# Kernel optimization log

Measured on AMD Instinct MI355X. Metric: run time of the kernel, lower is better.

Reference implementation:

```python
import jax, jax.numpy as jnp
import numpy as np

GRID_N = 256          # hardcoded 256x256 grid in the module
D = 64                # conv channel width
NL = 18               # module applications used (9 conv + 9 PReLU, interleaved)
LABEL_NC = 19
STYLE_DIM = 512


def setup_inputs() -> dict:
    key = jax.random.key(0)
    ks = jax.random.split(key, 7)
    B, C = 2, LABEL_NC
    x = jax.random.randint(ks[0], (B, C, GRID_N, GRID_N), 0, 2).astype(jnp.int32)
    conv_w0 = jax.random.normal(ks[1], (D, 2), dtype=jnp.float32) * 0.1
    conv_w = jax.random.normal(ks[2], (8, D, D), dtype=jnp.float32) * 0.05
    conv_b = jax.random.normal(ks[3], (9, D), dtype=jnp.float32) * 0.01
    prelu_a = jnp.full((9, D), 0.25, dtype=jnp.float32)  # PReLU default init
    fc_w = jax.random.normal(ks[4], (NL, STYLE_DIM, D * C), dtype=jnp.float32)
    fc_b = jnp.zeros((NL, STYLE_DIM), dtype=jnp.float32)
    return dict(x=x, conv_w0=conv_w0, conv_w=conv_w, conv_b=conv_b,
                prelu_a=prelu_a, fc_w=fc_w, fc_b=fc_b)


def _point_features(pts, conv_w0, conv_w, conv_b, prelu_a):
    """pts: (P,2). Returns (NL, P, D): snapshot after each of the 18 modules
    (conv, prelu, conv, prelu, ...) -- exactly what the original max-pools."""
    snaps = []
    z = pts @ conv_w0.T + conv_b[0]            # Conv1d(2,64,1) == pointwise linear
    snaps.append(z)
    z = jnp.where(z > 0, z, prelu_a[0] * z)    # PReLU(64)
    snaps.append(z)
    for i in range(8):
        z = z @ conv_w[i].T + conv_b[i + 1]
        snaps.append(z)
        z = jnp.where(z > 0, z, prelu_a[i + 1] * z)
        snaps.append(z)
    return jnp.stack(snaps)                    # (18, P, D)


def reference(x, conv_w0, conv_w, conv_b, prelu_a, fc_w, fc_b):
    B, C = x.shape[0], x.shape[1]
    P = GRID_N * GRID_N
    lin = jnp.linspace(-1.0, 1.0, GRID_N, dtype=jnp.float32)
    gx, gy = jnp.meshgrid(lin, lin)            # numpy default 'xy' indexing
    pts = jnp.stack([gx.reshape(-1), gy.reshape(-1)], axis=-1)   # (P, 2)

    # Grid points are shared by every (b, c): compute features once.
    snaps = _point_features(pts, conv_w0, conv_w, conv_b, prelu_a)        # (18, P, D)
    zero_snaps = _point_features(jnp.zeros((1, 2), jnp.float32),
                                 conv_w0, conv_w, conv_b, prelu_a)[:, 0]  # (18, D)

    mask = (x.reshape(B, C, P) == 1)           # (B, C, P)
    empty = ~jnp.any(mask, axis=-1)            # (B, C): original falls back to a zero point

    neg = jnp.float32(-jnp.inf)
    pooled = []
    for l in range(NL):                        # fixed, small layer loop
        pl = jnp.max(jnp.where(mask[..., None], snaps[l][None, None], neg), axis=2)  # (B,C,D)
        pl = jnp.where(empty[..., None], zero_snaps[l][None, None], pl)
        pooled.append(pl)
    pooled = jnp.stack(pooled, axis=1)         # (B, 18, C, D)
    feat = pooled.reshape(B, NL, C * D)        # channel-major concat, matches torch.cat dim=2

    # EqualLinear: out = x @ (W * scale).T + bias, scale = 1/sqrt(in_dim), lr_mul=1
    scale = 1.0 / jnp.sqrt(jnp.float32(C * D))
    # fcs are applied in reversed layer order and concatenated in that order
    w_rev = fc_w[::-1] * scale                 # (18, 512, C*D)
    b_rev = fc_b[::-1]                         # (18, 512)
    out = jnp.einsum('bld,lsd->bls', feat[:, ::-1], w_rev) + b_rev[None]
    return out                                  # (B, 18, 512)
```

## Files before the change

### kernel.cpp

```cpp
#include <hip/hip_runtime.h>
#include <hip/hip_fp16.h>

#define NSET 38
#define NSNAP 9
#define PART (NSNAP*NSET*64)
#define PPB 64
#define HSTR 72
#define PSTR 72
#define WHALF (8*64*64)

typedef unsigned int uint;
typedef __fp16 h2 __attribute__((ext_vector_type(2)));
typedef __fp16 h4 __attribute__((ext_vector_type(4)));
typedef __fp16 h8 __attribute__((ext_vector_type(8)));
typedef float  f32x4 __attribute__((ext_vector_type(4)));

#define HNEGINF 0xFC00u

static __device__ __forceinline__ h2 h2max(h2 a, h2 b) {
  return __builtin_elementwise_max(a, b);
}
#define SPLIT8(v, v0, v1, v2, v3)                       \
  h2 v0 = __builtin_shufflevector(v, v, 0, 1);          \
  h2 v1 = __builtin_shufflevector(v, v, 2, 3);          \
  h2 v2 = __builtin_shufflevector(v, v, 4, 5);          \
  h2 v3 = __builtin_shufflevector(v, v, 6, 7);

template<int CHUNKS>
__global__ __launch_bounds__(256)
void kA(const int* __restrict__ x, const float* __restrict__ w0,
        const float* __restrict__ cw, const float* __restrict__ cb,
        const float* __restrict__ pa, const __fp16* __restrict__ wf,
        __fp16* __restrict__ partialh)
{
  __shared__ __align__(16) __fp16 zth[PPB * HSTR];
  __shared__ __align__(16) __fp16 ztpA[64 * PSTR];
  __shared__ __align__(16) __fp16 ztpB[64 * PSTR];
  __shared__ __align__(16) __fp16 addp[40 * 64];
  __shared__ uint memb2[PPB * 2];

  const int tid = threadIdx.x;
  const int q  = tid & 63;
  const int g  = __builtin_amdgcn_readfirstlane(tid >> 6);
  const int lr = tid & 15;
  const int lg = (tid & 63) >> 4;
  const int sbase = g * 10;
  const int nset = (g == 3) ? 8 : 10;
  const __fp16 HNI = __builtin_bit_cast(__fp16, (unsigned short)0xFC00);
  const h2 H2NI = {HNI, HNI};

  auto prelu_frag = [&](int sv, f32x4* C, __fp16* ztpX) {
    #pragma unroll
    for (int dt = 0; dt < 4; ++dt) {
      int dim = (dt << 4) + lr;
      float a = pa[(sv << 6) + dim];
      __fp16 zp[4];
      #pragma unroll
      for (int r = 0; r < 4; ++r) {
        float zv = C[dt][r];
        zp[r] = (__fp16)(zv > 0.f ? zv : a * zv);
        zth[((g << 4) + (lg << 2) + r) * HSTR + dim] = zp[r];
      }
      int pt0 = (g << 4) + (lg << 2);
      h4 w4 = {zp[0], zp[1], zp[2], zp[3]};
      *(h4*)&ztpX[dim * PSTR + pt0] = w4;
    }
  };
  auto mfma_layer = [&](int sv, f32x4* C) {
    h8 a0 = *(const h8*)&zth[((g << 4) + lr) * HSTR + (lg << 3)];
    h8 a1 = *(const h8*)&zth[((g << 4) + lr) * HSTR + 32 + (lg << 3)];
    const __fp16* wb = wf + ((size_t)sv << 12);
    #pragma unroll
    for (int dt = 0; dt < 4; ++dt) {
      float bias = cb[((sv + 1) << 6) + (dt << 4) + lr];
      f32x4 a4 = {bias, bias, bias, bias};
      h8 b0 = *(const h8*)&wb[(((dt << 4) + lr) << 6) + (lg << 3)];
      h8 b1 = *(const h8*)&wb[(((dt << 4) + lr) << 6) + 32 + (lg << 3)];
      a4 = __builtin_amdgcn_mfma_f32_16x16x32_f16(a0, b0, a4, 0, 0, 0);
      a4 = __builtin_amdgcn_mfma_f32_16x16x32_f16(a1, b1, a4, 0, 0, 0);
      C[dt] = a4;
    }
  };
  auto fold_store = [&](int sv, h2* runv, int c) {
    __fp16* pb = partialh + (size_t)blockIdx.x * PART + sv * (NSET * 64) + q;
    #pragma unroll
    for (int j = 0; j < 10; ++j) {
      if (j < nset) {
        h2 r = runv[j];
        __fp16 m = r.x > r.y ? r.x : r.y;
        int off = (sbase + j) * 64;
        if (CHUNKS == 1 || c == 0) pb[off] = m;
        else { __fp16 o = pb[off]; pb[off] = (m > o) ? m : o; }
      }
    }
  };

  #pragma unroll 1
  for (int c = 0; c < CHUNKS; ++c) {
    const int p = (blockIdx.x * CHUNKS + c) * PPB + q;

    if (c) __syncthreads();
    if (tid < 128) {
      const int half = tid >> 6;
      uint m = 0;
      #pragma unroll
      for (int j = 0; j < 19; ++j)
        m |= (uint)(x[(half * 19 + j) * 65536 + p] == 1) << j;
      memb2[q * 2 + half] = m;
    }
    __syncthreads();

    {
      uint* addp32 = (uint*)addp;
      #pragma unroll
      for (int i = tid; i < 1280; i += 256) {
        int j = i >> 5, pr = i & 31;
        uint lo0 = memb2[(2 * pr) * 2],     hi0 = memb2[(2 * pr) * 2 + 1];
        uint lo1 = memb2[(2 * pr + 1) * 2], hi1 = memb2[(2 * pr + 1) * 2 + 1];
        uint b0 = (j < 19) ? ((lo0 >> j) & 1u) : (j < 38) ? ((hi0 >> (j - 19)) & 1u) : 0u;
        uint b1 = (j < 19) ? ((lo1 >> j) & 1u) : (j < 38) ? ((hi1 >> (j - 19)) & 1u) : 0u;
        addp32[i] = (b0 ? 0u : HNEGINF) | ((b1 ? 0u : HNEGINF) << 16);
      }
    }

    float acc0[16];
    {
      float px = -1.f + (2.f / 255.f) * (float)(p & 255);
      float py = -1.f + (2.f / 255.f) * (float)(p >> 8);
      #pragma unroll
      for (int d = 0; d < 16; ++d) {
        int dd = (g << 4) + d;
        acc0[d] = fmaf(px, w0[2 * dd], fmaf(py, w0[2 * dd + 1], cb[dd]));
      }
    }
    __syncthreads();

    #pragma unroll
    for (int d = 0; d < 16; ++d) {
      int dd = (g << 4) + d;
      float zv = acc0[d];
      float a = pa[dd];
      __fp16 zp = (__fp16)(zv > 0.f ? zv : a * zv);
      zth[q * HSTR + dd] = zp;
      ztpA[dd * PSTR + q] = zp;
    }
    __syncthreads();

    f32x4 Cf[4], Cf2[4];
    mfma_layer(0, Cf);

    {
      h2 runA[10];
      #pragma unroll
      for (int j = 0; j < 10; ++j) runA[j] = H2NI;
      #pragma unroll 2
      for (int c4 = 0; c4 < 8; ++c4) {
        h8 va = *(const h8*)&ztpA[q * PSTR + (c4 << 3)];
        SPLIT8(va, va0, va1, va2, va3)
        #pragma unroll
        for (int j = 0; j < 10; ++j) {
          h8 a8 = *(const h8*)&addp[((sbase + j) << 6) + (c4 << 3)];
          SPLIT8(a8, a0, a1, a2, a3)
          runA[j] = h2max(runA[j],
                     h2max(h2max(va0 + a0, va1 + a1), h2max(va2 + a2, va3 + a3)));
        }
      }
      fold_store(0, runA, c);
    }

    #pragma unroll 1
    for (int sp = 0; sp < 4; ++sp) {
      const int s = 1 + 2 * sp;
      __syncthreads();
      prelu_frag(s, Cf, ztpA);
      mfma_layer(s, Cf2);
      prelu_frag(s + 1, Cf2, ztpB);
      if (sp < 3) mfma_layer(s + 1, Cf);
      __syncthreads();

      h2 runA[10], runB[10];
      #pragma unroll
      for (int j = 0; j < 10; ++j) { runA[j] = H2NI; runB[j] = H2NI; }
      #pragma unroll 2
      for (int c4 = 0; c4 < 8; ++c4) {
        h8 va = *(const h8*)&ztpA[q * PSTR + (c4 << 3)];
        h8 vb = *(const h8*)&ztpB[q * PSTR + (c4 << 3)];
        SPLIT8(va, va0, va1, va2, va3)
        SPLIT8(vb, vb0, vb1, vb2, vb3)
        #pragma unroll
        for (int j = 0; j < 10; ++j) {
          h8 a8 = *(const h8*)&addp[((sbase + j) << 6) + (c4 << 3)];
          SPLIT8(a8, a0, a1, a2, a3)
          runA[j] = h2max(runA[j],
                     h2max(h2max(va0 + a0, va1 + a1), h2max(va2 + a2, va3 + a3)));
          runB[j] = h2max(runB[j],
                     h2max(h2max(vb0 + a0, vb1 + a1), h2max(vb2 + a2, vb3 + a3)));
        }
      }
      fold_store(s, runA, c);
      fold_store(s + 1, runB, c);
    }
  }
}

__global__ __launch_bounds__(256) void kW(const float* __restrict__ cw,
                                          __fp16* __restrict__ wf)
{
  int i = blockIdx.x * 256 + threadIdx.x;
  if (i < WHALF) wf[i] = (__fp16)cw[i];
}

__global__ __launch_bounds__(256) void kB1(const __fp16* __restrict__ ph,
    float* __restrict__ buf32, int per)
{
  int idx = blockIdx.x * 256 + threadIdx.x;
  if (idx >= PART) return;
  const __fp16* p0 = ph + (size_t)blockIdx.y * per * PART + idx;
  float mx = -3e38f;
  #pragma unroll 8
  for (int b = 0; b < per; ++b)
    mx = fmaxf(mx, (float)p0[(size_t)b * PART]);
  buf32[(size_t)blockIdx.y * PART + idx] = mx;
}

__global__ __launch_bounds__(256) void kB2(const float* __restrict__ buf32,
    const float* __restrict__ cw, const float* __restrict__ cb,
    const float* __restrict__ pa, float* __restrict__ feat)
{
  __shared__ float zl[64];
  __shared__ float zc[NSNAP][64];
  __shared__ float zp[NSNAP][64];
  int tid = threadIdx.x;
  int d = tid & 63;
  float z = cb[d];
  #pragma unroll 1
  for (int s = 0; s < NSNAP; ++s) {
    if (tid < 64) {
      zc[s][d] = z;
      float a = pa[(s << 6) + d];
      float v = z > 0.f ? z : a * z;
      zp[s][d] = v;
      zl[d] = v;
    }
    __syncthreads();
    if (s < 8) {
      if (tid < 64) {
        float a2 = cb[((s + 1) << 6) + d];
        for (int k = 0; k < 64; ++k)
          a2 = fmaf(zl[k], cw[(s << 12) + (d << 6) + k], a2);
        z = a2;
      }
    }
    __syncthreads();
  }

  int idx = blockIdx.x * 256 + tid;
  if (idx >= PART) return;
  int s = idx / (NSET * 64);
  int r = idx - s * (NSET * 64);
  int set = r >> 6;
  int dd = r & 63;
  float mx = -3e38f;
  #pragma unroll
  for (int y = 0; y < 32; ++y)
    mx = fmaxf(mx, buf32[(size_t)y * PART + idx]);
  int b = set / 19, cc = set - b * 19;
  float even_v, odd_v;
  if (mx < -5e37f) {
    even_v = zc[s][dd];
    odd_v  = zp[s][dd];
  } else {
    odd_v = mx;
    float a = pa[(s << 6) + dd];
    even_v = mx > 0.f ? mx : mx / a;
  }
  size_t fb = ((size_t)b * 18 + 2 * s) * 1216 + cc * 64 + dd;
  feat[fb] = even_v;
  feat[fb + 1216] = odd_v;
}

__global__ __launch_bounds__(256) void kC(const float* __restrict__ feat,
    const float* __restrict__ fcw, const float* __restrict__ fcb,
    float* __restrict__ out)
{
  __shared__ float f0[1216], f1[1216];
  int lr = blockIdx.y;
  int chunk = blockIdx.x;
  int tid = threadIdx.x;
  for (int i = tid; i < 1216; i += 256) {
    f0[i] = feat[(size_t)(0 * 18 + lr) * 1216 + i];
    f1[i] = feat[(size_t)(1 * 18 + lr) * 1216 + i];
  }
  __syncthreads();
  int wv = tid >> 6, lane = tid & 63;
  float scale = 1.f / sqrtf(1216.f);
  int l = 17 - lr;
  #pragma unroll 1
  for (int rr = 0; rr < 4; ++rr) {
    int srow = (chunk << 4) + (wv << 2) + rr;
    const float* wrow = fcw + ((size_t)lr * 512 + srow) * 1216;
    float pp0 = 0.f, pp1 = 0.f;
    #pragma unroll
    for (int k = 0; k < 19; ++k) {
      float w = wrow[(k << 6) + lane];
      pp0 = fmaf(w, f0[(k << 6) + lane], pp0);
      pp1 = fmaf(w, f1[(k << 6) + lane], pp1);
    }
    #pragma unroll
    for (int off = 32; off; off >>= 1) {
      pp0 += __shfl_xor(pp0, off, 64);
      pp1 += __shfl_xor(pp1, off, 64);
    }
    if (lane == 0) {
      float b = fcb[lr * 512 + srow];
      out[((size_t)0 * 18 + l) * 512 + srow] = fmaf(scale, pp0, b);
      out[((size_t)1 * 18 + l) * 512 + srow] = fmaf(scale, pp1, b);
    }
  }
}

extern "C" void kernel_launch(void* const* d_in, const int* in_sizes, int n_in,
                              void* d_out, int out_size, void* d_ws, size_t ws_size,
                              hipStream_t stream) {
  const int*   x   = (const int*)d_in[0];
  const float* w0  = (const float*)d_in[1];
  const float* cw  = (const float*)d_in[2];
  const float* cb  = (const float*)d_in[3];
  const float* pa  = (const float*)d_in[4];
  const float* fcw = (const float*)d_in[5];
  const float* fcb = (const float*)d_in[6];
  float* out = (float*)d_out;
  char* base = (char*)d_ws;

  #define NEED(n) ((size_t)(n) * PART * 2 + (size_t)32 * PART * 4 \
                   + (size_t)2 * 18 * 1216 * 4 + (size_t)WHALF * 2)

  int nblk;
  if      (ws_size >= NEED(1024)) nblk = 1024;
  else if (ws_size >= NEED(512))  nblk = 512;
  else                            nblk = 256;

  __fp16* partialh = (__fp16*)base;
  float*  buf32 = (float*)(base + (size_t)nblk * PART * 2);
  float*  feat  = buf32 + (size_t)32 * PART;
  __fp16* wf    = (__fp16*)(feat + (size_t)2 * 18 * 1216);
  const int per = nblk >> 5;

  hipLaunchKernelGGL(kW, dim3(WHALF / 256), dim3(256), 0, stream, cw, wf);

  if (nblk == 1024) {
    hipLaunchKernelGGL(kA<1>, dim3(1024), dim3(256), 0, stream,
                       x, w0, cw, cb, pa, wf, partialh);
  } else if (nblk == 512) {
    hipLaunchKernelGGL(kA<2>, dim3(512), dim3(256), 0, stream,
                       x, w0, cw, cb, pa, wf, partialh);
  } else {
    hipLaunchKernelGGL(kA<4>, dim3(256), dim3(256), 0, stream,
                       x, w0, cw, cb, pa, wf, partialh);
  }

  hipLaunchKernelGGL(kB1, dim3(86, 32), dim3(256), 0, stream,
                     partialh, buf32, per);
  hipLaunchKernelGGL(kB2, dim3(86), dim3(256), 0, stream,
                     buf32, cw, cb, pa, feat);
  hipLaunchKernelGGL(kC, dim3(32, 18), dim3(256), 0, stream, feat, fcw, fcb, out);
}
```

Baseline: 133.3 us.

## Pool three snapshots per pass with packed-f16 asm and grid-stride chunks

```diff
diff --git a/kernel.cpp b/kernel.cpp
--- a/kernel.cpp
+++ b/kernel.cpp
@@ -5,28 +5,31 @@
 #define NSNAP 9
 #define PART (NSNAP*NSET*64)
 #define PPB 64
+#define NCHUNK 1024
 #define HSTR 72
 #define PSTR 72
 #define WHALF (8*64*64)
 
 typedef unsigned int uint;
-typedef __fp16 h2 __attribute__((ext_vector_type(2)));
-typedef __fp16 h4 __attribute__((ext_vector_type(4)));
 typedef __fp16 h8 __attribute__((ext_vector_type(8)));
 typedef float  f32x4 __attribute__((ext_vector_type(4)));
 
 #define HNEGINF 0xFC00u
-
-static __device__ __forceinline__ h2 h2max(h2 a, h2 b) {
-  return __builtin_elementwise_max(a, b);
-}
-#define SPLIT8(v, v0, v1, v2, v3)                       \
-  h2 v0 = __builtin_shufflevector(v, v, 0, 1);          \
-  h2 v1 = __builtin_shufflevector(v, v, 2, 3);          \
-  h2 v2 = __builtin_shufflevector(v, v, 4, 5);          \
-  h2 v3 = __builtin_shufflevector(v, v, 6, 7);
-
-template<int CHUNKS>
+#define NEGPACK (HNEGINF | (HNEGINF << 16))
+
+static __device__ __forceinline__ uint pk_add(uint a, uint b) {
+  uint r; asm("v_pk_add_f16 %0, %1, %2" : "=v"(r) : "v"(a), "v"(b)); return r;
+}
+static __device__ __forceinline__ void pk_max_acc(uint& acc, uint t) {
+  asm("v_pk_max_f16 %0, %1, %0" : "+v"(acc) : "v"(t));
+}
+static __device__ __forceinline__ float half_lo_f(uint u) {
+  return (float)__builtin_bit_cast(__fp16, (unsigned short)(u & 0xFFFFu));
+}
+static __device__ __forceinline__ float half_hi_f(uint u) {
+  return (float)__builtin_bit_cast(__fp16, (unsigned short)(u >> 16));
+}
+
 __global__ __launch_bounds__(256)
 void kA(const int* __restrict__ x, const float* __restrict__ w0,
         const float* __restrict__ cw, const float* __restrict__ cb,
@@ -36,6 +39,7 @@
   __shared__ __align__(16) __fp16 zth[PPB * HSTR];
   __shared__ __align__(16) __fp16 ztpA[64 * PSTR];
   __shared__ __align__(16) __fp16 ztpB[64 * PSTR];
+  __shared__ __align__(16) __fp16 ztpC[64 * PSTR];
   __shared__ __align__(16) __fp16 addp[40 * 64];
   __shared__ uint memb2[PPB * 2];
 
@@ -46,8 +50,6 @@
   const int lg = (tid & 63) >> 4;
   const int sbase = g * 10;
   const int nset = (g == 3) ? 8 : 10;
-  const __fp16 HNI = __builtin_bit_cast(__fp16, (unsigned short)0xFC00);
-  const h2 H2NI = {HNI, HNI};
 
   auto prelu_frag = [&](int sv, f32x4* C, __fp16* ztpX) {
     #pragma unroll
@@ -62,8 +64,12 @@
         zth[((g << 4) + (lg << 2) + r) * HSTR + dim] = zp[r];
       }
       int pt0 = (g << 4) + (lg << 2);
-      h4 w4 = {zp[0], zp[1], zp[2], zp[3]};
-      *(h4*)&ztpX[dim * PSTR + pt0] = w4;
+      uint2 w2;
+      w2.x = (uint)__builtin_bit_cast(unsigned short, zp[0]) |
+             ((uint)__builtin_bit_cast(unsigned short, zp[1]) << 16);
+      w2.y = (uint)__builtin_bit_cast(unsigned short, zp[2]) |
+             ((uint)__builtin_bit_cast(unsigned short, zp[3]) << 16);
+      *(uint2*)&ztpX[dim * PSTR + pt0] = w2;
     }
   };
   auto mfma_layer = [&](int sv, f32x4* C) {
@@ -81,25 +87,57 @@
       C[dt] = a4;
     }
   };
-  auto fold_store = [&](int sv, h2* runv, int c) {
+  auto fold_store = [&](int sv, uint* runv, bool first) {
     __fp16* pb = partialh + (size_t)blockIdx.x * PART + sv * (NSET * 64) + q;
     #pragma unroll
     for (int j = 0; j < 10; ++j) {
       if (j < nset) {
-        h2 r = runv[j];
-        __fp16 m = r.x > r.y ? r.x : r.y;
+        __fp16 lo = __builtin_bit_cast(__fp16, (unsigned short)(runv[j] & 0xFFFFu));
+        __fp16 hi = __builtin_bit_cast(__fp16, (unsigned short)(runv[j] >> 16));
+        __fp16 m = lo > hi ? lo : hi;
         int off = (sbase + j) * 64;
-        if (CHUNKS == 1 || c == 0) pb[off] = m;
+        if (first) pb[off] = m;
         else { __fp16 o = pb[off]; pb[off] = (m > o) ? m : o; }
       }
     }
   };
+  auto pool3 = [&](int sa, bool first) {
+    uint runA[10], runB[10], runC[10];
+    #pragma unroll
+    for (int j = 0; j < 10; ++j) { runA[j] = NEGPACK; runB[j] = NEGPACK; runC[j] = NEGPACK; }
+    #pragma unroll 2
+    for (int c4 = 0; c4 < 8; ++c4) {
+      uint4 va = *(const uint4*)&ztpA[q * PSTR + (c4 << 3)];
+      uint4 vb = *(const uint4*)&ztpB[q * PSTR + (c4 << 3)];
+      uint4 vc = *(const uint4*)&ztpC[q * PSTR + (c4 << 3)];
+      #pragma unroll
+      for (int j = 0; j < 10; ++j) {
+        uint4 aj = *(const uint4*)&addp[((sbase + j) << 6) + (c4 << 3)];
+        pk_max_acc(runA[j], pk_add(va.x, aj.x));
+        pk_max_acc(runA[j], pk_add(va.y, aj.y));
+        pk_max_acc(runA[j], pk_add(va.z, aj.z));
+        pk_max_acc(runA[j], pk_add(va.w, aj.w));
+        pk_max_acc(runB[j], pk_add(vb.x, aj.x));
+        pk_max_acc(runB[j], pk_add(vb.y, aj.y));
+        pk_max_acc(runB[j], pk_add(vb.z, aj.z));
+        pk_max_acc(runB[j], pk_add(vb.w, aj.w));
+        pk_max_acc(runC[j], pk_add(vc.x, aj.x));
+        pk_max_acc(runC[j], pk_add(vc.y, aj.y));
+        pk_max_acc(runC[j], pk_add(vc.z, aj.z));
+        pk_max_acc(runC[j], pk_add(vc.w, aj.w));
+      }
+    }
+    fold_store(sa, runA, first);
+    fold_store(sa + 1, runB, first);
+    fold_store(sa + 2, runC, first);
+  };
 
   #pragma unroll 1
-  for (int c = 0; c < CHUNKS; ++c) {
-    const int p = (blockIdx.x * CHUNKS + c) * PPB + q;
-
-    if (c) __syncthreads();
+  for (int cid = blockIdx.x; cid < NCHUNK; cid += gridDim.x) {
+    const bool first = (cid == (int)blockIdx.x);
+    const int p = cid * PPB + q;
+
+    if (!first) __syncthreads();
     if (tid < 128) {
       const int half = tid >> 6;
       uint m = 0;
@@ -146,60 +184,33 @@
     }
     __syncthreads();
 
-    f32x4 Cf[4], Cf2[4];
-    mfma_layer(0, Cf);
-
-    {
-      h2 runA[10];
-      #pragma unroll
-      for (int j = 0; j < 10; ++j) runA[j] = H2NI;
-      #pragma unroll 2
-      for (int c4 = 0; c4 < 8; ++c4) {
-        h8 va = *(const h8*)&ztpA[q * PSTR + (c4 << 3)];
-        SPLIT8(va, va0, va1, va2, va3)
-        #pragma unroll
-        for (int j = 0; j < 10; ++j) {
-          h8 a8 = *(const h8*)&addp[((sbase + j) << 6) + (c4 << 3)];
-          SPLIT8(a8, a0, a1, a2, a3)
-          runA[j] = h2max(runA[j],
-                     h2max(h2max(va0 + a0, va1 + a1), h2max(va2 + a2, va3 + a3)));
-        }
-      }
-      fold_store(0, runA, c);
-    }
-
-    #pragma unroll 1
-    for (int sp = 0; sp < 4; ++sp) {
-      const int s = 1 + 2 * sp;
-      __syncthreads();
-      prelu_frag(s, Cf, ztpA);
-      mfma_layer(s, Cf2);
-      prelu_frag(s + 1, Cf2, ztpB);
-      if (sp < 3) mfma_layer(s + 1, Cf);
-      __syncthreads();
-
-      h2 runA[10], runB[10];
-      #pragma unroll
-      for (int j = 0; j < 10; ++j) { runA[j] = H2NI; runB[j] = H2NI; }
-      #pragma unroll 2
-      for (int c4 = 0; c4 < 8; ++c4) {
-        h8 va = *(const h8*)&ztpA[q * PSTR + (c4 << 3)];
-        h8 vb = *(const h8*)&ztpB[q * PSTR + (c4 << 3)];
-        SPLIT8(va, va0, va1, va2, va3)
-        SPLIT8(vb, vb0, vb1, vb2, vb3)
-        #pragma unroll
-        for (int j = 0; j < 10; ++j) {
-          h8 a8 = *(const h8*)&addp[((sbase + j) << 6) + (c4 << 3)];
-          SPLIT8(a8, a0, a1, a2, a3)
-          runA[j] = h2max(runA[j],
-                     h2max(h2max(va0 + a0, va1 + a1), h2max(va2 + a2, va3 + a3)));
-          runB[j] = h2max(runB[j],
-                     h2max(h2max(vb0 + a0, vb1 + a1), h2max(vb2 + a2, vb3 + a3)));
-        }
-      }
-      fold_store(s, runA, c);
-      fold_store(s + 1, runB, c);
-    }
+    f32x4 CfA[4], CfB[4];
+    mfma_layer(0, CfA);
+    prelu_frag(1, CfA, ztpB);
+    mfma_layer(1, CfB);
+    prelu_frag(2, CfB, ztpC);
+    mfma_layer(2, CfA);
+    __syncthreads();
+    pool3(0, first);
+
+    __syncthreads();
+    prelu_frag(3, CfA, ztpA);
+    mfma_layer(3, CfB);
+    prelu_frag(4, CfB, ztpB);
+    mfma_layer(4, CfA);
+    prelu_frag(5, CfA, ztpC);
+    mfma_layer(5, CfB);
+    __syncthreads();
+    pool3(3, first);
+
+    __syncthreads();
+    prelu_frag(6, CfB, ztpA);
+    mfma_layer(6, CfA);
+    prelu_frag(7, CfA, ztpB);
+    mfma_layer(7, CfB);
+    prelu_frag(8, CfB, ztpC);
+    __syncthreads();
+    pool3(6, first);
   }
 }
 
@@ -336,9 +347,9 @@
                    + (size_t)2 * 18 * 1216 * 4 + (size_t)WHALF * 2)
 
   int nblk;
-  if      (ws_size >= NEED(1024)) nblk = 1024;
-  else if (ws_size >= NEED(512))  nblk = 512;
-  else                            nblk = 256;
+  if      (ws_size >= NEED(768)) nblk = 768;
+  else if (ws_size >= NEED(512)) nblk = 512;
+  else                           nblk = 256;
 
   __fp16* partialh = (__fp16*)base;
   float*  buf32 = (float*)(base + (size_t)nblk * PART * 2);
@@ -347,18 +358,8 @@
   const int per = nblk >> 5;
 
   hipLaunchKernelGGL(kW, dim3(WHALF / 256), dim3(256), 0, stream, cw, wf);
-
-  if (nblk == 1024) {
-    hipLaunchKernelGGL(kA<1>, dim3(1024), dim3(256), 0, stream,
-                       x, w0, cw, cb, pa, wf, partialh);
-  } else if (nblk == 512) {
-    hipLaunchKernelGGL(kA<2>, dim3(512), dim3(256), 0, stream,
-                       x, w0, cw, cb, pa, wf, partialh);
-  } else {
-    hipLaunchKernelGGL(kA<4>, dim3(256), dim3(256), 0, stream,
-                       x, w0, cw, cb, pa, wf, partialh);
-  }
-
+  hipLaunchKernelGGL(kA, dim3(nblk), dim3(256), 0, stream,
+                     x, w0, cw, cb, pa, wf, partialh);
   hipLaunchKernelGGL(kB1, dim3(86, 32), dim3(256), 0, stream,
                      partialh, buf32, per);
   hipLaunchKernelGGL(kB2, dim3(86), dim3(256), 0, stream,
```

Measured after the change: 239.0 us. 1.79x slower.
